# Kernel tuning notes

Measured on AMD Instinct MI355X. Metric: run time of the kernel, lower is better.

Reference implementation:

```python
import jax, jax.numpy as jnp
import numpy as np

B, S, D, K = 16, 4096, 256, 1024


def setup_inputs() -> dict:
    key = jax.random.key(0)
    k1, k2 = jax.random.split(key)
    z_e = jax.random.normal(k1, (B, S, D), dtype=jnp.float32)
    # nn.Embedding weight initialized uniform(-1/K, 1/K)
    codebook = jax.random.uniform(k2, (K, D), dtype=jnp.float32,
                                  minval=-1.0 / K, maxval=1.0 / K)
    return {"z_e": z_e, "codebook": codebook}


def reference(z_e, codebook):
    # straight_through path of VQEmbedding
    d = codebook.shape[1]
    x = z_e.reshape(-1, d)                                   # [N, D]
    dist = (jnp.sum(x * x, axis=1, keepdims=True)
            + jnp.sum(codebook * codebook, axis=1)
            - 2.0 * (x @ codebook.T))                        # [N, K]
    idx = jnp.argmin(dist, axis=1)                           # [N]
    codes = jnp.take(codebook, idx, axis=0).reshape(z_e.shape)  # gather
    z_q = z_e + jax.lax.stop_gradient(codes - z_e)           # straight-through codes (detached codebook)
    z_q_bar = codes                                          # codes with grad to codebook
    return (z_q, z_q_bar)
```

## Files before the change

kernel.cpp:

```cpp
#include <hip/hip_runtime.h>
#include <stdint.h>

#define D 256
#define KCODES 1024
#define NROWS 65536

using int4v  = __attribute__((ext_vector_type(4))) int;
using f32x4v = __attribute__((ext_vector_type(4))) float;

__device__ __forceinline__ float rne_f(float x) { return __builtin_rintf(x); }

__device__ __forceinline__ void gl_lds16(const void* g, void* l) {
  __builtin_amdgcn_global_load_lds(
      (const __attribute__((address_space(1))) void*)g,
      (__attribute__((address_space(3))) void*)l, 16, 0, 0);
}

__device__ __forceinline__ void dig4(float t, int* d) {
  float f0 = rne_f(t);  float t1 = __fmul_rn(__fsub_rn(t, f0), 256.0f);
  float f1 = rne_f(t1); float t2 = __fmul_rn(__fsub_rn(t1, f1), 256.0f);
  float f2 = rne_f(t2); float t3 = __fmul_rn(__fsub_rn(t2, f2), 256.0f);
  float f3 = rne_f(t3);
  int d0 = (int)f0, d1 = (int)f1, d2 = (int)f2, d3 = (int)f3;
  if (d3 == 128) { d3 = -128; ++d2; }
  if (d2 == 128) { d2 = -128; ++d1; }
  if (d1 == 128) { d1 = -128; ++d0; }
  d[0] = d0; d[1] = d1; d[2] = d2; d[3] = d3;
}

__device__ __forceinline__ float np_block128_sumsq(const float* __restrict__ q) {
  float r[8], v[8];
  *(float4*)(v) = *(const float4*)(q);
  *(float4*)(v + 4) = *(const float4*)(q + 4);
#pragma unroll
  for (int j = 0; j < 8; ++j) r[j] = __fmul_rn(v[j], v[j]);
  for (int i = 8; i < 128; i += 8) {
    *(float4*)(v) = *(const float4*)(q + i);
    *(float4*)(v + 4) = *(const float4*)(q + i + 4);
#pragma unroll
    for (int j = 0; j < 8; ++j) r[j] = __fadd_rn(r[j], __fmul_rn(v[j], v[j]));
  }
  float t01 = __fadd_rn(r[0], r[1]);
  float t23 = __fadd_rn(r[2], r[3]);
  float t45 = __fadd_rn(r[4], r[5]);
  float t67 = __fadd_rn(r[6], r[7]);
  return __fadd_rn(__fadd_rn(t01, t23), __fadd_rn(t45, t67));
}
__device__ __forceinline__ float np_sumsq256(const float* __restrict__ q) {
  return __fadd_rn(np_block128_sumsq(q), np_block128_sumsq(q + 128));
}

__global__ __launch_bounds__(256) void prep_all(const float* __restrict__ z,
                                                const float* __restrict__ cb,
                                                float* __restrict__ c2,
                                                float* __restrict__ srow,
                                                char* __restrict__ cbd) {
  __shared__ float zs[64][260];
  const int bid = blockIdx.x;
  const int tid = threadIdx.x;
  if (bid < 1040) {
    const float* src; float* dst; int r0;
    if (bid < 1024) { r0 = bid * 64; src = z; dst = srow; }
    else            { r0 = (bid - 1024) * 64; src = cb; dst = c2; }
#pragma unroll
    for (int it = 0; it < 16; ++it) {
      int g = tid + it * 256, row = g >> 6, f4 = g & 63;
      *(float4*)(&zs[row][f4 * 4]) = *(const float4*)(src + (size_t)(r0 + row) * D + f4 * 4);
    }
    __syncthreads();
    if (tid < 64) dst[r0 + tid] = np_sumsq256(&zs[tid][0]);
    return;
  }
  int id = (bid - 1040) * 256 + tid;
  int n = id >> 4, kc = id & 15;
  int f = kc >> 2, kg = kc & 3, nt = n >> 5, c = n & 31;
  const float* src = cb + (size_t)n * D + kc * 16;
  float v[16];
  *(float4*)(v) = *(const float4*)(src);
  *(float4*)(v + 4) = *(const float4*)(src + 4);
  *(float4*)(v + 8) = *(const float4*)(src + 8);
  *(float4*)(v + 12) = *(const float4*)(src + 12);
  int dg[16][4];
#pragma unroll
  for (int e = 0; e < 16; ++e) dig4(v[e] * 65536.0f, dg[e]);
  size_t base = (size_t)nt * 8192 + f * 2048 + (c >> 4) * 1024 + kg * 256 + (c & 15) * 16;
#pragma unroll
  for (int p = 0; p < 4; ++p) {
    int4v wv;
#pragma unroll
    for (int wi = 0; wi < 4; ++wi)
      wv[wi] = (dg[wi * 4][p] & 255) | ((dg[wi * 4 + 1][p] & 255) << 8) |
               ((dg[wi * 4 + 2][p] & 255) << 16) | (dg[wi * 4 + 3][p] << 24);
    *(int4v*)(cbd + (size_t)p * (KCODES * 256) + base) = wv;
  }
}

#define BM 128
#define BN 16
#define NT (KCODES / BN)

#define MFI16(a, b, c) __builtin_amdgcn_mfma_i32_16x16x64_i8((a), (b), (c), 0, 0, 0)

__global__ __launch_bounds__(256, 2) void vq_mfma(
    const float* __restrict__ z, const float* __restrict__ cb,
    const float* __restrict__ c2g, const float* __restrict__ srowg,
    const char* __restrict__ cbd, float* __restrict__ out) {
  __shared__ alignas(16) char bbuf[2][16384];
  __shared__ float c2s[KCODES];
  __shared__ int bidx_s[BM];

  const int tid = threadIdx.x;
  const int lane = tid & 63;
  const int w = tid >> 6;
  const int r0 = blockIdx.x * BM;
  const int l15 = lane & 15, l4 = lane >> 4;

  c2s[tid] = c2g[tid];
  c2s[tid + 256] = c2g[tid + 256];
  c2s[tid + 512] = c2g[tid + 512];
  c2s[tid + 768] = c2g[tid + 768];

  float sr[8];
#pragma unroll
  for (int fi = 0; fi < 2; ++fi)
#pragma unroll
    for (int r = 0; r < 4; ++r)
      sr[fi * 4 + r] = srowg[r0 + w * 32 + fi * 16 + l4 * 4 + r];

  int4v AdA[4][4], AdB[4][4];
#pragma unroll
  for (int fi = 0; fi < 2; ++fi) {
    const float* zr0 = z + (size_t)(r0 + w * 32 + fi * 16 + l15) * D + l4 * 16;
#pragma unroll
    for (int f = 0; f < 4; ++f) {
      float v[16];
      *(float4*)(v) = *(const float4*)(zr0 + f * 64);
      *(float4*)(v + 4) = *(const float4*)(zr0 + f * 64 + 4);
      *(float4*)(v + 8) = *(const float4*)(zr0 + f * 64 + 8);
      *(float4*)(v + 12) = *(const float4*)(zr0 + f * 64 + 12);
      int dg[16][4];
#pragma unroll
      for (int e = 0; e < 16; ++e) dig4(v[e] * 16.0f, dg[e]);
#pragma unroll
      for (int p = 0; p < 4; ++p) {
        int4v wv;
#pragma unroll
        for (int wi = 0; wi < 4; ++wi)
          wv[wi] = (dg[wi * 4][p] & 255) | ((dg[wi * 4 + 1][p] & 255) << 8) |
                   ((dg[wi * 4 + 2][p] & 255) << 16) | (dg[wi * 4 + 3][p] << 24);
        if (fi == 0) AdA[p][f] = wv; else AdB[p][f] = wv;
      }
    }
  }

  const char* cbd_b = cbd;
#define STAGE(ntv, dstbase) do { \
    const char* s_ = cbd_b + (size_t)((ntv) >> 1) * 8192 + (tid >> 6) * 2048 + \
                     ((ntv) & 1) * 1024 + (tid & 63) * 16; \
    char* d_ = (dstbase) + (tid >> 6) * 1024 + (tid & 63) * 16; \
    gl_lds16(s_,          d_); \
    gl_lds16(s_ + 262144, d_ + 4096); \
    gl_lds16(s_ + 524288, d_ + 8192); \
    gl_lds16(s_ + 786432, d_ + 12288); \
  } while (0)

#define LOADB(set, basep, kf) do { \
    const char* pk_ = (basep) + (kf) * 1024; \
    B0##set = *(const int4v*)(pk_); \
    B1##set = *(const int4v*)(pk_ + 4096); \
    B2##set = *(const int4v*)(pk_ + 8192); \
    B3##set = *(const int4v*)(pk_ + 12288); \
  } while (0)

#define CLUSTER2(set, kf) do { \
    accA[1] = MFI16(AdA[0][kf], B1##set, accA[1]); \
    accB[1] = MFI16(AdB[0][kf], B1##set, accB[1]); \
    accA[3] = MFI16(AdA[0][kf], B3##set, accA[3]); \
    accB[3] = MFI16(AdB[0][kf], B3##set, accB[3]); \
    accA[2] = MFI16(AdA[0][kf], B2##set, accA[2]); \
    accB[2] = MFI16(AdB[0][kf], B2##set, accB[2]); \
    accA[1] = MFI16(AdA[1][kf], B0##set, accA[1]); \
    accB[1] = MFI16(AdB[1][kf], B0##set, accB[1]); \
    accA[3] = MFI16(AdA[1][kf], B2##set, accA[3]); \
    accB[3] = MFI16(AdB[1][kf], B2##set, accB[3]); \
    accA[2] = MFI16(AdA[1][kf], B1##set, accA[2]); \
    accB[2] = MFI16(AdB[1][kf], B1##set, accB[2]); \
    accA[0] = MFI16(AdA[0][kf], B0##set, accA[0]); \
    accB[0] = MFI16(AdB[0][kf], B0##set, accB[0]); \
    accA[3] = MFI16(AdA[2][kf], B1##set, accA[3]); \
    accB[3] = MFI16(AdB[2][kf], B1##set, accB[3]); \
    accA[2] = MFI16(AdA[2][kf], B0##set, accA[2]); \
    accB[2] = MFI16(AdB[2][kf], B0##set, accB[2]); \
    accA[3] = MFI16(AdA[3][kf], B0##set, accA[3]); \
    accB[3] = MFI16(AdB[3][kf], B0##set, accB[3]); \
  } while (0)

#define CLUSTER20(set) do { \
    accA[1] = MFI16(AdA[0][0], B1##set, ZZ); \
    accB[1] = MFI16(AdB[0][0], B1##set, ZZ); \
    accA[3] = MFI16(AdA[0][0], B3##set, ZZ); \
    accB[3] = MFI16(AdB[0][0], B3##set, ZZ); \
    accA[2] = MFI16(AdA[0][0], B2##set, ZZ); \
    accB[2] = MFI16(AdB[0][0], B2##set, ZZ); \
    accA[1] = MFI16(AdA[1][0], B0##set, accA[1]); \
    accB[1] = MFI16(AdB[1][0], B0##set, accB[1]); \
    accA[3] = MFI16(AdA[1][0], B2##set, accA[3]); \
    accB[3] = MFI16(AdB[1][0], B2##set, accB[3]); \
    accA[2] = MFI16(AdA[1][0], B1##set, accA[2]); \
    accB[2] = MFI16(AdB[1][0], B1##set, accB[2]); \
    accA[0] = MFI16(AdA[0][0], B0##set, ZZ); \
    accB[0] = MFI16(AdB[0][0], B0##set, ZZ); \
    accA[3] = MFI16(AdA[2][0], B1##set, accA[3]); \
    accB[3] = MFI16(AdB[2][0], B1##set, accB[3]); \
    accA[2] = MFI16(AdA[2][0], B0##set, accA[2]); \
    accB[2] = MFI16(AdB[2][0], B0##set, accB[2]); \
    accA[3] = MFI16(AdA[3][0], B0##set, accA[3]); \
    accB[3] = MFI16(AdB[3][0], B0##set, accB[3]); \
  } while (0)

  float bd[8]; int bi[8];
#pragma unroll
  for (int r = 0; r < 8; ++r) { bd[r] = 3.4e38f; bi[r] = 0x7fffffff; }

  const int4v ZZ = {0, 0, 0, 0};
  int4v accA[4], accB[4];
  int4v B0a, B1a, B2a, B3a;
  int4v B0b, B1b, B2b, B3b;

  STAGE(0, &bbuf[0][0]);
  __syncthreads();

  for (int nt = 0; nt < NT; ++nt) {
    const char* basep = &bbuf[nt & 1][0] + lane * 16;
    if (nt + 1 < NT) STAGE(nt + 1, &bbuf[(nt + 1) & 1][0]);

    LOADB(a, basep, 0);
    LOADB(b, basep, 1);
    CLUSTER20(a);
    LOADB(a, basep, 2);
    CLUSTER2(b, 1);
    LOADB(b, basep, 3);
    CLUSTER2(a, 2);
    CLUSTER2(b, 3);

    {
      const int kc = nt * BN + l15;
      const float c2v = c2s[kc];
#pragma unroll
      for (int r = 0; r < 4; ++r) {
        int hi32 = accA[0][r] * 256 + accA[1][r];
        double lo_d = fma((double)accA[2][r], 256.0, (double)accA[3][r]);
        float mf2 = (float)(fma((double)hi32, 65536.0, lo_d) * 0x1p-43);
        float dist = __fsub_rn(__fadd_rn(sr[r], c2v), mf2);
        if (dist < bd[r]) { bd[r] = dist; bi[r] = kc; }
      }
#pragma unroll
      for (int r = 0; r < 4; ++r) {
        int hi32 = accB[0][r] * 256 + accB[1][r];
        double lo_d = fma((double)accB[2][r], 256.0, (double)accB[3][r]);
        float mf2 = (float)(fma((double)hi32, 65536.0, lo_d) * 0x1p-43);
        float dist = __fsub_rn(__fadd_rn(sr[4 + r], c2v), mf2);
        if (dist < bd[4 + r]) { bd[4 + r] = dist; bi[4 + r] = kc; }
      }
    }
    __syncthreads();
  }

#pragma unroll
  for (int r = 0; r < 8; ++r) {
#pragma unroll
    for (int m = 1; m < 16; m <<= 1) {
      float od = __shfl_xor(bd[r], m);
      int oi = __shfl_xor(bi[r], m);
      if (od < bd[r] || (od == bd[r] && oi < bi[r])) { bd[r] = od; bi[r] = oi; }
    }
    if (l15 == 0) bidx_s[w * 32 + (r >> 2) * 16 + l4 * 4 + (r & 3)] = bi[r];
  }
  __syncthreads();

  {
    float* out0 = out;
    float* out1 = out + (size_t)NROWS * D;
#pragma unroll
    for (int rr = 0; rr < 32; ++rr) {
      const int row_l = w * 32 + rr;
      const int grow = r0 + row_l;
      const int kb = bidx_s[row_l];
      f32x4v c4 = *(const f32x4v*)(cb + (size_t)kb * D + lane * 4);
      f32x4v z4 = *(const f32x4v*)(z + (size_t)grow * D + lane * 4);
      f32x4v q;
      q.x = __fadd_rn(z4.x, __fsub_rn(c4.x, z4.x));
      q.y = __fadd_rn(z4.y, __fsub_rn(c4.y, z4.y));
      q.z = __fadd_rn(z4.z, __fsub_rn(c4.z, z4.z));
      q.w = __fadd_rn(z4.w, __fsub_rn(c4.w, z4.w));
      __builtin_nontemporal_store(q, (f32x4v*)(out0 + (size_t)grow * D + lane * 4));
      __builtin_nontemporal_store(c4, (f32x4v*)(out1 + (size_t)grow * D + lane * 4));
    }
  }
}

__global__ void c2_kernel_fb(const float* __restrict__ cb, float* __restrict__ c2) {
  int k = blockIdx.x * blockDim.x + threadIdx.x;
  if (k < KCODES) c2[k] = np_sumsq256(cb + (size_t)k * D);
}

__global__ __launch_bounds__(256) void vq_fallback(const float* __restrict__ z,
                                                   const float* __restrict__ cb,
                                                   const float* __restrict__ c2,
                                                   float* __restrict__ out) {
  __shared__ float zs[64][260];
  __shared__ float cs[64][260];
  __shared__ float srow[64];
  __shared__ int bidx[64];
  const int tid = threadIdx.x;
  const int tx = tid & 15, ty = tid >> 4;
  const int r0 = blockIdx.x * 64;
#pragma unroll
  for (int it = 0; it < 16; ++it) {
    int g = tid + it * 256, row = g >> 6, f4 = g & 63;
    *(float4*)(&zs[row][f4 * 4]) = *(const float4*)(z + (size_t)(r0 + row) * D + f4 * 4);
  }
  __syncthreads();
  if (tid < 64) srow[tid] = np_sumsq256(&zs[tid][0]);
  float bd[4]; int bi[4];
#pragma unroll
  for (int j = 0; j < 4; ++j) { bd[j] = 3.4e38f; bi[j] = 0x7fffffff; }
  for (int t = 0; t < KCODES / 64; ++t) {
    __syncthreads();
#pragma unroll
    for (int it = 0; it < 16; ++it) {
      int g = tid + it * 256, row = g >> 6, f4 = g & 63;
      *(float4*)(&cs[row][f4 * 4]) = *(const float4*)(cb + (size_t)(t * 64 + row) * D + f4 * 4);
    }
    __syncthreads();
    double acc[4][4];
#pragma unroll
    for (int j = 0; j < 4; ++j)
#pragma unroll
      for (int i = 0; i < 4; ++i) acc[j][i] = 0.0;
#pragma unroll 2
    for (int d = 0; d < D; d += 4) {
      float4 a[4], b[4];
#pragma unroll
      for (int j = 0; j < 4; ++j) a[j] = *(const float4*)(&zs[ty + 16 * j][d]);
#pragma unroll
      for (int i = 0; i < 4; ++i) b[i] = *(const float4*)(&cs[tx + 16 * i][d]);
#pragma unroll
      for (int j = 0; j < 4; ++j)
#pragma unroll
        for (int i = 0; i < 4; ++i) {
          acc[j][i] += (double)a[j].x * (double)b[i].x;
          acc[j][i] += (double)a[j].y * (double)b[i].y;
          acc[j][i] += (double)a[j].z * (double)b[i].z;
          acc[j][i] += (double)a[j].w * (double)b[i].w;
        }
    }
#pragma unroll
    for (int j = 0; j < 4; ++j) {
      const float s = srow[ty + 16 * j];
#pragma unroll
      for (int i = 0; i < 4; ++i) {
        const int k = t * 64 + tx + 16 * i;
        const float m = (float)acc[j][i];
        const float dist = __fsub_rn(__fadd_rn(s, c2[k]), __fmul_rn(2.0f, m));
        if (dist < bd[j]) { bd[j] = dist; bi[j] = k; }
      }
    }
  }
  __syncthreads();
  float* red_d = &cs[0][0];
  int* red_i = (int*)&cs[20][0];
#pragma unroll
  for (int j = 0; j < 4; ++j) {
    red_d[(ty + 16 * j) * 16 + tx] = bd[j];
    red_i[(ty + 16 * j) * 16 + tx] = bi[j];
  }
  __syncthreads();
  if (tid < 64) {
    float best = red_d[tid * 16 + 0];
    int bsti = red_i[tid * 16 + 0];
    for (int x = 1; x < 16; ++x) {
      float d2 = red_d[tid * 16 + x]; int i2 = red_i[tid * 16 + x];
      if (d2 < best || (d2 == best && i2 < bsti)) { best = d2; bsti = i2; }
    }
    bidx[tid] = bsti;
  }
  __syncthreads();
  const int wid = tid >> 6, lane = tid & 63;
  float* out0 = out;
  float* out1 = out + (size_t)NROWS * D;
  for (int r = wid; r < 64; r += 4) {
    const int gr = r0 + r;
    const int kb = bidx[r];
    float4 c4 = *(const float4*)(cb + (size_t)kb * D + lane * 4);
    float4 z4 = *(const float4*)(&zs[r][lane * 4]);
    float4 q;
    q.x = __fadd_rn(z4.x, __fsub_rn(c4.x, z4.x));
    q.y = __fadd_rn(z4.y, __fsub_rn(c4.y, z4.y));
    q.z = __fadd_rn(z4.z, __fsub_rn(c4.z, z4.z));
    q.w = __fadd_rn(z4.w, __fsub_rn(c4.w, z4.w));
    *(float4*)(out0 + (size_t)gr * D + lane * 4) = q;
    *(float4*)(out1 + (size_t)gr * D + lane * 4) = c4;
  }
}

extern "C" void kernel_launch(void* const* d_in, const int* in_sizes, int n_in,
                              void* d_out, int out_size, void* d_ws, size_t ws_size,
                              hipStream_t stream) {
  const float* z = (const float*)d_in[0];
  const float* cb = (const float*)d_in[1];
  float* out = (float*)d_out;

  const size_t c2_off = 0;
  const size_t srow_off = 4096;
  const size_t cbd_off = 4096 + 262144;
  const size_t need = cbd_off + (size_t)4 * KCODES * 256;

  if (ws_size < need) {
    float* c2 = (float*)d_ws;
    c2_kernel_fb<<<KCODES / 256, 256, 0, stream>>>(cb, c2);
    vq_fallback<<<NROWS / 64, 256, 0, stream>>>(z, cb, c2, out);
    return;
  }

  float* c2 = (float*)((char*)d_ws + c2_off);
  float* srow = (float*)((char*)d_ws + srow_off);
  char* cbd = (char*)d_ws + cbd_off;

  prep_all<<<1104, 256, 0, stream>>>(z, cb, c2, srow, cbd);
  vq_mfma<<<NROWS / BM, 256, 0, stream>>>(z, cb, c2, srow, cbd, out);
}
```

Baseline: 167.5 us.

## Software-pipeline distance epilogue with next tile's MFMA using double accumulators

Splits the accumulators into two ping-pong sets (P/Q) and manually unrolls the codebook-tile loop by two. Each tile's integer-to-distance conversion and argmin update is deferred into the middle of the next tile's MFMA sequence, so the VALU/FP64 epilogue can overlap matrix work. This doubles accumulator register use, which may raise register pressure and lower occupancy. It also assumes NT is even for the prologue/loop/epilogue split.

```diff
diff --git a/kernel.cpp b/kernel.cpp
--- a/kernel.cpp
+++ b/kernel.cpp
@@ -172,98 +172,142 @@
     B3##set = *(const int4v*)(pk_ + 12288); \
   } while (0)
 
-#define CLUSTER2(set, kf) do { \
-    accA[1] = MFI16(AdA[0][kf], B1##set, accA[1]); \
-    accB[1] = MFI16(AdB[0][kf], B1##set, accB[1]); \
-    accA[3] = MFI16(AdA[0][kf], B3##set, accA[3]); \
-    accB[3] = MFI16(AdB[0][kf], B3##set, accB[3]); \
-    accA[2] = MFI16(AdA[0][kf], B2##set, accA[2]); \
-    accB[2] = MFI16(AdB[0][kf], B2##set, accB[2]); \
-    accA[1] = MFI16(AdA[1][kf], B0##set, accA[1]); \
-    accB[1] = MFI16(AdB[1][kf], B0##set, accB[1]); \
-    accA[3] = MFI16(AdA[1][kf], B2##set, accA[3]); \
-    accB[3] = MFI16(AdB[1][kf], B2##set, accB[3]); \
-    accA[2] = MFI16(AdA[1][kf], B1##set, accA[2]); \
-    accB[2] = MFI16(AdB[1][kf], B1##set, accB[2]); \
-    accA[0] = MFI16(AdA[0][kf], B0##set, accA[0]); \
-    accB[0] = MFI16(AdB[0][kf], B0##set, accB[0]); \
-    accA[3] = MFI16(AdA[2][kf], B1##set, accA[3]); \
-    accB[3] = MFI16(AdB[2][kf], B1##set, accB[3]); \
-    accA[2] = MFI16(AdA[2][kf], B0##set, accA[2]); \
-    accB[2] = MFI16(AdB[2][kf], B0##set, accB[2]); \
-    accA[3] = MFI16(AdA[3][kf], B0##set, accA[3]); \
-    accB[3] = MFI16(AdB[3][kf], B0##set, accB[3]); \
+#define CLUSTER2S(S, set, kf) do { \
+    accA##S[1] = MFI16(AdA[0][kf], B1##set, accA##S[1]); \
+    accB##S[1] = MFI16(AdB[0][kf], B1##set, accB##S[1]); \
+    accA##S[3] = MFI16(AdA[0][kf], B3##set, accA##S[3]); \
+    accB##S[3] = MFI16(AdB[0][kf], B3##set, accB##S[3]); \
+    accA##S[2] = MFI16(AdA[0][kf], B2##set, accA##S[2]); \
+    accB##S[2] = MFI16(AdB[0][kf], B2##set, accB##S[2]); \
+    accA##S[1] = MFI16(AdA[1][kf], B0##set, accA##S[1]); \
+    accB##S[1] = MFI16(AdB[1][kf], B0##set, accB##S[1]); \
+    accA##S[3] = MFI16(AdA[1][kf], B2##set, accA##S[3]); \
+    accB##S[3] = MFI16(AdB[1][kf], B2##set, accB##S[3]); \
+    accA##S[2] = MFI16(AdA[1][kf], B1##set, accA##S[2]); \
+    accB##S[2] = MFI16(AdB[1][kf], B1##set, accB##S[2]); \
+    accA##S[0] = MFI16(AdA[0][kf], B0##set, accA##S[0]); \
+    accB##S[0] = MFI16(AdB[0][kf], B0##set, accB##S[0]); \
+    accA##S[3] = MFI16(AdA[2][kf], B1##set, accA##S[3]); \
+    accB##S[3] = MFI16(AdB[2][kf], B1##set, accB##S[3]); \
+    accA##S[2] = MFI16(AdA[2][kf], B0##set, accA##S[2]); \
+    accB##S[2] = MFI16(AdB[2][kf], B0##set, accB##S[2]); \
+    accA##S[3] = MFI16(AdA[3][kf], B0##set, accA##S[3]); \
+    accB##S[3] = MFI16(AdB[3][kf], B0##set, accB##S[3]); \
   } while (0)
 
-#define CLUSTER20(set) do { \
-    accA[1] = MFI16(AdA[0][0], B1##set, ZZ); \
-    accB[1] = MFI16(AdB[0][0], B1##set, ZZ); \
-    accA[3] = MFI16(AdA[0][0], B3##set, ZZ); \
-    accB[3] = MFI16(AdB[0][0], B3##set, ZZ); \
-    accA[2] = MFI16(AdA[0][0], B2##set, ZZ); \
-    accB[2] = MFI16(AdB[0][0], B2##set, ZZ); \
-    accA[1] = MFI16(AdA[1][0], B0##set, accA[1]); \
-    accB[1] = MFI16(AdB[1][0], B0##set, accB[1]); \
-    accA[3] = MFI16(AdA[1][0], B2##set, accA[3]); \
-    accB[3] = MFI16(AdB[1][0], B2##set, accB[3]); \
-    accA[2] = MFI16(AdA[1][0], B1##set, accA[2]); \
-    accB[2] = MFI16(AdB[1][0], B1##set, accB[2]); \
-    accA[0] = MFI16(AdA[0][0], B0##set, ZZ); \
-    accB[0] = MFI16(AdB[0][0], B0##set, ZZ); \
-    accA[3] = MFI16(AdA[2][0], B1##set, accA[3]); \
-    accB[3] = MFI16(AdB[2][0], B1##set, accB[3]); \
-    accA[2] = MFI16(AdA[2][0], B0##set, accA[2]); \
-    accB[2] = MFI16(AdB[2][0], B0##set, accB[2]); \
-    accA[3] = MFI16(AdA[3][0], B0##set, accA[3]); \
-    accB[3] = MFI16(AdB[3][0], B0##set, accB[3]); \
+#define CLUSTER20S(S, set) do { \
+    accA##S[1] = MFI16(AdA[0][0], B1##set, ZZ); \
+    accB##S[1] = MFI16(AdB[0][0], B1##set, ZZ); \
+    accA##S[3] = MFI16(AdA[0][0], B3##set, ZZ); \
+    accB##S[3] = MFI16(AdB[0][0], B3##set, ZZ); \
+    accA##S[2] = MFI16(AdA[0][0], B2##set, ZZ); \
+    accB##S[2] = MFI16(AdB[0][0], B2##set, ZZ); \
+    accA##S[1] = MFI16(AdA[1][0], B0##set, accA##S[1]); \
+    accB##S[1] = MFI16(AdB[1][0], B0##set, accB##S[1]); \
+    accA##S[3] = MFI16(AdA[1][0], B2##set, accA##S[3]); \
+    accB##S[3] = MFI16(AdB[1][0], B2##set, accB##S[3]); \
+    accA##S[2] = MFI16(AdA[1][0], B1##set, accA##S[2]); \
+    accB##S[2] = MFI16(AdB[1][0], B1##set, accB##S[2]); \
+    accA##S[0] = MFI16(AdA[0][0], B0##set, ZZ); \
+    accB##S[0] = MFI16(AdB[0][0], B0##set, ZZ); \
+    accA##S[3] = MFI16(AdA[2][0], B1##set, accA##S[3]); \
+    accB##S[3] = MFI16(AdB[2][0], B1##set, accB##S[3]); \
+    accA##S[2] = MFI16(AdA[2][0], B0##set, accA##S[2]); \
+    accB##S[2] = MFI16(AdB[2][0], B0##set, accB##S[2]); \
+    accA##S[3] = MFI16(AdA[3][0], B0##set, accA##S[3]); \
+    accB##S[3] = MFI16(AdB[3][0], B0##set, accB##S[3]); \
   } while (0)
 
+#define FIN(S, tt) do { \
+    const int kc_ = (tt) * BN + l15; \
+    const float c2v_ = c2s[kc_]; \
+    _Pragma("unroll") \
+    for (int r = 0; r < 4; ++r) { \
+      int hi32 = accA##S[0][r] * 256 + accA##S[1][r]; \
+      double lo_d = fma((double)accA##S[2][r], 256.0, (double)accA##S[3][r]); \
+      float mf2 = (float)(fma((double)hi32, 65536.0, lo_d) * 0x1p-43); \
+      float dist = __fsub_rn(__fadd_rn(sr[r], c2v_), mf2); \
+      if (dist < bd[r]) { bd[r] = dist; bi[r] = kc_; } \
+    } \
+    _Pragma("unroll") \
+    for (int r = 0; r < 4; ++r) { \
+      int hi32 = accB##S[0][r] * 256 + accB##S[1][r]; \
+      double lo_d = fma((double)accB##S[2][r], 256.0, (double)accB##S[3][r]); \
+      float mf2 = (float)(fma((double)hi32, 65536.0, lo_d) * 0x1p-43); \
+      float dist = __fsub_rn(__fadd_rn(sr[4 + r], c2v_), mf2); \
+      if (dist < bd[4 + r]) { bd[4 + r] = dist; bi[4 + r] = kc_; } \
+    } \
+  } while (0)
+
   float bd[8]; int bi[8];
 #pragma unroll
   for (int r = 0; r < 8; ++r) { bd[r] = 3.4e38f; bi[r] = 0x7fffffff; }
 
   const int4v ZZ = {0, 0, 0, 0};
-  int4v accA[4], accB[4];
+  int4v accAP[4], accBP[4], accAQ[4], accBQ[4];
   int4v B0a, B1a, B2a, B3a;
   int4v B0b, B1b, B2b, B3b;
 
   STAGE(0, &bbuf[0][0]);
   __syncthreads();
 
-  for (int nt = 0; nt < NT; ++nt) {
-    const char* basep = &bbuf[nt & 1][0] + lane * 16;
-    if (nt + 1 < NT) STAGE(nt + 1, &bbuf[(nt + 1) & 1][0]);
-
+  {
+    const char* basep = &bbuf[0][0] + lane * 16;
+    STAGE(1, &bbuf[1][0]);
     LOADB(a, basep, 0);
     LOADB(b, basep, 1);
-    CLUSTER20(a);
+    CLUSTER20S(P, a);
     LOADB(a, basep, 2);
-    CLUSTER2(b, 1);
+    CLUSTER2S(P, b, 1);
     LOADB(b, basep, 3);
-    CLUSTER2(a, 2);
-    CLUSTER2(b, 3);
-
+    CLUSTER2S(P, a, 2);
+    CLUSTER2S(P, b, 3);
+    __syncthreads();
+  }
+
+  for (int t = 1; t + 1 < NT; t += 2) {
     {
-      const int kc = nt * BN + l15;
-      const float c2v = c2s[kc];
-#pragma unroll
-      for (int r = 0; r < 4; ++r) {
-        int hi32 = accA[0][r] * 256 + accA[1][r];
-        double lo_d = fma((double)accA[2][r], 256.0, (double)accA[3][r]);
-        float mf2 = (float)(fma((double)hi32, 65536.0, lo_d) * 0x1p-43);
-        float dist = __fsub_rn(__fadd_rn(sr[r], c2v), mf2);
-        if (dist < bd[r]) { bd[r] = dist; bi[r] = kc; }
-      }
-#pragma unroll
-      for (int r = 0; r < 4; ++r) {
-        int hi32 = accB[0][r] * 256 + accB[1][r];
-        double lo_d = fma((double)accB[2][r], 256.0, (double)accB[3][r]);
-        float mf2 = (float)(fma((double)hi32, 65536.0, lo_d) * 0x1p-43);
-        float dist = __fsub_rn(__fadd_rn(sr[4 + r], c2v), mf2);
-        if (dist < bd[4 + r]) { bd[4 + r] = dist; bi[4 + r] = kc; }
-      }
-    }
-    __syncthreads();
+      const char* basep = &bbuf[1][0] + lane * 16;
+      STAGE(t + 1, &bbuf[0][0]);
+      LOADB(a, basep, 0);
+      LOADB(b, basep, 1);
+      CLUSTER20S(Q, a);
+      LOADB(a, basep, 2);
+      CLUSTER2S(Q, b, 1);
+      FIN(P, t - 1);
+      LOADB(b, basep, 3);
+      CLUSTER2S(Q, a, 2);
+      CLUSTER2S(Q, b, 3);
+      __syncthreads();
+    }
+    {
+      const char* basep = &bbuf[0][0] + lane * 16;
+      STAGE(t + 2, &bbuf[1][0]);
+      LOADB(a, basep, 0);
+      LOADB(b, basep, 1);
+      CLUSTER20S(P, a);
+      LOADB(a, basep, 2);
+      CLUSTER2S(P, b, 1);
+      FIN(Q, t);
+      LOADB(b, basep, 3);
+      CLUSTER2S(P, a, 2);
+      CLUSTER2S(P, b, 3);
+      __syncthreads();
+    }
+  }
+
+  {
+    const char* basep = &bbuf[1][0] + lane * 16;
+    LOADB(a, basep, 0);
+    LOADB(b, basep, 1);
+    CLUSTER20S(Q, a);
+    LOADB(a, basep, 2);
+    CLUSTER2S(Q, b, 1);
+    FIN(P, NT - 2);
+    LOADB(b, basep, 3);
+    CLUSTER2S(Q, a, 2);
+    CLUSTER2S(Q, b, 3);
+    FIN(Q, NT - 1);
   }
 
 #pragma unroll
```

Measured after the change: 248.4 us. +48.2%, slower.
